# Optimization experiments

Measured on AMD Instinct MI355X. Metric: run time of the kernel, lower is better.

## Reference

```python
import jax, jax.numpy as jnp
import numpy as np

NEG = -1.0e9


def setup_inputs() -> dict:
    key = jax.random.key(0)
    ks = jax.random.split(key, 8)
    B, L, D = 4, 2048, 1024
    s = 1.0 / np.sqrt(D)
    return {
        "x": jax.random.normal(ks[0], (B, L, D), dtype=jnp.float32),
        "Wq": jax.random.normal(ks[1], (D, D), dtype=jnp.float32) * s,
        "bq": jax.random.normal(ks[2], (D,), dtype=jnp.float32) * 0.02,
        "Wk": jax.random.normal(ks[3], (D, D), dtype=jnp.float32) * s,
        "bk": jax.random.normal(ks[4], (D,), dtype=jnp.float32) * 0.02,
        "Wv": jax.random.normal(ks[5], (D, D), dtype=jnp.float32) * s,
        "bv": jax.random.normal(ks[6], (D,), dtype=jnp.float32) * 0.02,
        "lengths": jax.random.randint(ks[7], (B,), 1, 2048, dtype=jnp.int32),
    }


def reference(x, Wq, bq, Wk, bk, Wv, bv, lengths):
    # x: [B, L, D]; single-head self-attention with causal + length additive masks
    B, L, D = x.shape
    q = x @ Wq + bq  # [B, L, D]
    k = x @ Wk + bk
    v = x @ Wv + bv
    scale = 1.0 / jnp.sqrt(jnp.asarray(D, dtype=x.dtype))
    att = jnp.einsum("bid,bjd->bij", q, k) * scale  # [B, L, L]
    idx = jnp.arange(L)
    causal = jnp.where(idx[None, :] > idx[:, None], NEG, 0.0).astype(x.dtype)  # [L, L]
    # length mask: NEG where j >= len[b] or i >= len[b]
    invalid = (idx[None, :] >= lengths[:, None])  # [B, L]
    lenmask = jnp.where(invalid[:, :, None] | invalid[:, None, :], NEG, 0.0).astype(x.dtype)
    att = att + causal[None, :, :] + lenmask
    att = jax.nn.softmax(att, axis=-1)
    return jnp.einsum("bij,bjd->bid", att, v)
```

## Files before the change

kernel.cpp:

```cpp
#include <hip/hip_runtime.h>

#define NEGV (-1.0e9f)

typedef __bf16 bf16_t;
typedef __bf16 bf16x8 __attribute__((ext_vector_type(8)));
typedef __bf16 bf16x4 __attribute__((ext_vector_type(4)));
typedef float  f32x4  __attribute__((ext_vector_type(4)));

__device__ __forceinline__ void gld16(const void* g, void* l) {
    __builtin_amdgcn_global_load_lds(
        (const __attribute__((address_space(1))) void*)g,
        (__attribute__((address_space(3))) void*)l, 16, 0, 0);
}


#define MMR(AF, IB)                                                                        \
    acc[IB][0] = __builtin_amdgcn_mfma_f32_16x16x32_bf16(AF, b0, acc[IB][0], 0, 0, 0);     \
    acc[IB][1] = __builtin_amdgcn_mfma_f32_16x16x32_bf16(AF, b1, acc[IB][1], 0, 0, 0);     \
    acc[IB][2] = __builtin_amdgcn_mfma_f32_16x16x32_bf16(AF, b2, acc[IB][2], 0, 0, 0);     \
    acc[IB][3] = __builtin_amdgcn_mfma_f32_16x16x32_bf16(AF, b3, acc[IB][3], 0, 0, 0)

__device__ __forceinline__ void ml128x128(
    const bf16_t* __restrict__ A, const bf16_t* __restrict__ B,
    int ldA, int ldB, int nkt, char* smem, int tid, f32x4 acc[4][4])
{
    const int w = tid >> 6, lane = tid & 63;
    const int wm = w & 1, wn = w >> 1;
    const int l16 = lane & 15, quad = lane >> 4;

    const int g0 = 2 * (tid >> 3) + ((tid >> 2) & 1);
    const int c0 = ((tid & 3) ^ ((tid >> 3) & 3)) * 8;
    const bf16_t* pa0 = A + (size_t)g0 * ldA + c0;
    const bf16_t* pa1 = pa0 + (size_t)64 * ldA;
    const bf16_t* pb0 = B + (size_t)g0 * ldB + c0;
    const bf16_t* pb1 = pb0 + (size_t)64 * ldB;
    char* const stA = smem + (w << 10);
    char* const stB = smem + 24576 + (w << 10);

    const int rowo = (l16 >> 1) * 128 + (l16 & 1) * 64 + ((quad ^ ((l16 >> 1) & 3)) << 4);
    const char* rdA = smem + (wm << 12) + rowo;
    const char* rdB = smem + 24576 + (wn << 12) + rowo;

#define STG4(BO) do { gld16(pa0, stA + (BO)); gld16(pa1, stA + (BO) + 4096);   \
                      gld16(pb0, stB + (BO)); gld16(pb1, stB + (BO) + 4096);   \
                      pa0 += 32; pa1 += 32; pb0 += 32; pb1 += 32; } while (0)

    STG4(0);
    if (nkt > 1) {
        STG4(8192);
        asm volatile("s_waitcnt vmcnt(4)" ::: "memory");
    } else {
        asm volatile("s_waitcnt vmcnt(0)" ::: "memory");
    }
    __builtin_amdgcn_s_barrier();

    int ro = 0, so = 16384;
    for (int kt = 0; kt < nkt; ++kt) {
        const char* ra = rdA + ro;
        const char* rb = rdB + ro;
        bf16x8 a0 = *(const bf16x8*)(ra);
        bf16x8 a1 = *(const bf16x8*)(ra + 1024);
        bf16x8 a2 = *(const bf16x8*)(ra + 2048);
        bf16x8 a3 = *(const bf16x8*)(ra + 3072);
        bf16x8 b0 = *(const bf16x8*)(rb);
        bf16x8 b1 = *(const bf16x8*)(rb + 1024);
        bf16x8 b2 = *(const bf16x8*)(rb + 2048);
        bf16x8 b3 = *(const bf16x8*)(rb + 3072);
        const bool st = (kt + 2) < nkt;
        if (st) STG4(so);
        asm volatile("s_waitcnt lgkmcnt(0)" ::: "memory");
        __builtin_amdgcn_sched_barrier(0);
        __builtin_amdgcn_s_setprio(1);
        MMR(a0, 0); MMR(a1, 1); MMR(a2, 2); MMR(a3, 3);
        __builtin_amdgcn_s_setprio(0);
        if (st) asm volatile("s_waitcnt vmcnt(4)" ::: "memory");
        else    asm volatile("s_waitcnt vmcnt(0)" ::: "memory");
        __builtin_amdgcn_s_barrier();
        ro = (ro == 16384) ? 0 : (ro + 8192);
        so = (so == 16384) ? 0 : (so + 8192);
    }
#undef STG4
}

__global__ __launch_bounds__(256)
void convert_x_kernel(const float* __restrict__ x, bf16_t* __restrict__ xb)
{
    const size_t i = ((size_t)blockIdx.x * 256 + threadIdx.x) * 8;
    float4 a = *(const float4*)&x[i];
    float4 b = *(const float4*)&x[i + 4];
    bf16x8 o;
    o[0] = (bf16_t)a.x; o[1] = (bf16_t)a.y; o[2] = (bf16_t)a.z; o[3] = (bf16_t)a.w;
    o[4] = (bf16_t)b.x; o[5] = (bf16_t)b.y; o[6] = (bf16_t)b.z; o[7] = (bf16_t)b.w;
    *(bf16x8*)&xb[i] = o;
}

__global__ __launch_bounds__(256)
void transpose_w_kernel(const float* __restrict__ W0, const float* __restrict__ W1,
                        const float* __restrict__ W2, bf16_t* __restrict__ WT)
{
    __shared__ float t[32][33];
    const float* W = (blockIdx.z == 0) ? W0 : (blockIdx.z == 1) ? W1 : W2;
    bf16_t* WTz = WT + (size_t)blockIdx.z * 1024 * 1024;
    const int k0 = blockIdx.y * 32, n0 = blockIdx.x * 32;
    const int r = threadIdx.x >> 3, c4 = (threadIdx.x & 7) * 4;
    float4 v = *(const float4*)&W[(size_t)(k0 + r) * 1024 + n0 + c4];
    t[r][c4 + 0] = v.x; t[r][c4 + 1] = v.y; t[r][c4 + 2] = v.z; t[r][c4 + 3] = v.w;
    __syncthreads();
    bf16x4 o;
#pragma unroll
    for (int j = 0; j < 4; ++j) o[j] = (bf16_t)t[c4 + j][r];
    *(bf16x4*)&WTz[(size_t)(n0 + r) * 1024 + k0 + c4] = o;
}

__global__ __launch_bounds__(256)
void gemm_qk128(const bf16_t* __restrict__ A, const bf16_t* __restrict__ Bt,
                const float* __restrict__ bq, const float* __restrict__ bk,
                bf16_t* __restrict__ C, int N, int Kd)
{
    __shared__ __align__(16) char smem[49152];
    int bid = blockIdx.y * 16 + blockIdx.x;
    bid = (bid & 7) * 128 + (bid >> 3);
    const int n0 = (bid & 15) << 7;
    const int m0 = (bid >> 4) << 7;
    const int tid = threadIdx.x;

    f32x4 acc[4][4];
#pragma unroll
    for (int i = 0; i < 4; ++i)
#pragma unroll
        for (int j = 0; j < 4; ++j) acc[i][j] = (f32x4)(0.0f);

    ml128x128(A + (size_t)m0 * Kd, Bt + (size_t)n0 * Kd, Kd, Kd, Kd >> 5,
              smem, tid, acc);

    const int w = tid >> 6, lane = tid & 63;
    const int wm = w & 1, wn = w >> 1, quad = lane >> 4, l16 = lane & 15;
#pragma unroll
    for (int j = 0; j < 4; ++j) {
        const int col = n0 + wn * 64 + j * 16 + l16;
        const float bval = (col < 1024) ? bq[col] : bk[col - 1024];
#pragma unroll
        for (int i = 0; i < 4; ++i) {
            const int row = m0 + wm * 64 + i * 16 + quad * 4;
#pragma unroll
            for (int r = 0; r < 4; ++r)
                C[(size_t)(row + r) * N + col] = (bf16_t)(acc[i][j][r] + bval);
        }
    }
}

__global__ __launch_bounds__(256)
void gemm_vt128(const bf16_t* __restrict__ WvT, const bf16_t* __restrict__ xb,
                const float* __restrict__ bv, bf16_t* __restrict__ VT,
                int N, int Kd)
{
    __shared__ __align__(16) char smem[49152];
    int bid = blockIdx.y * 64 + blockIdx.x;
    bid = (bid & 7) * 64 + (bid >> 3);
    const int m0 = (bid >> 6) << 7;
    const int n0 = (bid & 63) << 7;
    const int tid = threadIdx.x;

    f32x4 acc[4][4];
#pragma unroll
    for (int i = 0; i < 4; ++i)
#pragma unroll
        for (int j = 0; j < 4; ++j) acc[i][j] = (f32x4)(0.0f);

    ml128x128(WvT + (size_t)m0 * Kd, xb + (size_t)n0 * Kd, Kd, Kd, Kd >> 5,
              smem, tid, acc);

    const int w = tid >> 6, lane = tid & 63;
    const int wm = w & 1, wn = w >> 1, quad = lane >> 4, l16 = lane & 15;
#pragma unroll
    for (int i = 0; i < 4; ++i) {
        const int row = m0 + wm * 64 + i * 16 + quad * 4;
#pragma unroll
        for (int r = 0; r < 4; ++r) {
            const float bval = bv[row + r];
#pragma unroll
            for (int j = 0; j < 4; ++j) {
                const int col = n0 + wn * 64 + j * 16 + l16;
                VT[(size_t)(row + r) * N + col] = (bf16_t)(acc[i][j][r] + bval);
            }
        }
    }
}

__global__ __launch_bounds__(256)
void scores128(const bf16_t* __restrict__ Q, const bf16_t* __restrict__ K,
               int ldq, const int* __restrict__ lengths,
               bf16_t* __restrict__ U, float2* __restrict__ stats,
               int L, int Dd, float alpha)
{
    __shared__ __align__(16) char smem[49152];
    const int b = blockIdx.z;
    const int len = lengths[b];
    int tix = (int)blockIdx.x;
    tix = (tix & 7) * 17 + (tix >> 3);
    int it = 0;
    while ((it + 1) * (it + 2) / 2 <= tix) ++it;
    const int jt = tix - it * (it + 1) / 2;
    const int m0 = it << 7, n0 = jt << 7;
    const int tid = threadIdx.x;

    f32x4 acc[4][4];
#pragma unroll
    for (int i = 0; i < 4; ++i)
#pragma unroll
        for (int j = 0; j < 4; ++j) acc[i][j] = (f32x4)(0.0f);

    const bf16_t* Qb = Q + (size_t)b * L * ldq + (size_t)m0 * ldq;
    const bf16_t* Kb = K + (size_t)b * L * ldq + (size_t)n0 * ldq;
    ml128x128(Qb, Kb, ldq, ldq, Dd >> 5, smem, tid, acc);

    const int w = tid >> 6, lane = tid & 63;
    const int wm = w & 1, wn = w >> 1, quad = lane >> 4, l16 = lane & 15;
    bf16_t* Ub = U + (size_t)b * L * L;
    float2* strow = stats + (size_t)b * L * 32;
    const int chnk = (n0 >> 6) + wn;
#pragma unroll
    for (int i = 0; i < 4; ++i) {
#pragma unroll
        for (int r = 0; r < 4; ++r) {
            const int row = m0 + wm * 64 + i * 16 + quad * 4 + r;
            float sv[4];
#pragma unroll
            for (int j = 0; j < 4; ++j) {
                const int col = n0 + wn * 64 + j * 16 + l16;
                float v = acc[i][j][r] * alpha;
                if (col > row) v += NEGV;
                if (row >= len || col >= len) v += NEGV;
                sv[j] = v;
            }
            float m = fmaxf(fmaxf(sv[0], sv[1]), fmaxf(sv[2], sv[3]));
            m = fmaxf(m, __shfl_xor(m, 1, 64));
            m = fmaxf(m, __shfl_xor(m, 2, 64));
            m = fmaxf(m, __shfl_xor(m, 4, 64));
            m = fmaxf(m, __shfl_xor(m, 8, 64));
            float ssum = 0.f;
#pragma unroll
            for (int j = 0; j < 4; ++j) {
                sv[j] = __expf(sv[j] - m);
                ssum += sv[j];
            }
            ssum += __shfl_xor(ssum, 1, 64);
            ssum += __shfl_xor(ssum, 2, 64);
            ssum += __shfl_xor(ssum, 4, 64);
            ssum += __shfl_xor(ssum, 8, 64);
#pragma unroll
            for (int j = 0; j < 4; ++j)
                Ub[(size_t)row * L + n0 + wn * 64 + j * 16 + l16] = (bf16_t)sv[j];
            if (l16 == 0) strow[(size_t)row * 32 + chnk] = make_float2(m, ssum);
        }
    }
}

__global__ __launch_bounds__(256)
void sm_finalize_norm(const float2* __restrict__ stats, bf16_t* __restrict__ U,
                      int L)
{
    __shared__ float sc[32];
    const int i = blockIdx.x;
    const int bound = ((i >> 7) + 1) << 7;
    const int nch = bound >> 6;
    const size_t base = ((size_t)blockIdx.y * L + i) * 32;
    const int t = threadIdx.x;

    if (t < 32) {
        float m_c = -3.0e38f, s_c = 0.f;
        if (t < nch) { float2 st = stats[base + t]; m_c = st.x; s_c = st.y; }
        float M = m_c;
        M = fmaxf(M, __shfl_xor(M, 1, 64));
        M = fmaxf(M, __shfl_xor(M, 2, 64));
        M = fmaxf(M, __shfl_xor(M, 4, 64));
        M = fmaxf(M, __shfl_xor(M, 8, 64));
        M = fmaxf(M, __shfl_xor(M, 16, 64));
        const float e = __expf(m_c - M);
        float d = s_c * e;
        d += __shfl_xor(d, 1, 64);
        d += __shfl_xor(d, 2, 64);
        d += __shfl_xor(d, 4, 64);
        d += __shfl_xor(d, 8, 64);
        d += __shfl_xor(d, 16, 64);
        sc[t] = e / d;
    }
    __syncthreads();

    const int j8 = t * 8;
    if (j8 < bound) {
        bf16_t* row = U + ((size_t)blockIdx.y * L + i) * L;
        bf16x8 u = *(const bf16x8*)&row[j8];
        const float c = sc[t >> 3];
        bf16x8 o;
#pragma unroll
        for (int j = 0; j < 8; ++j) o[j] = (bf16_t)((float)u[j] * c);
        *(bf16x8*)&row[j8] = o;
    }
}

__global__ __launch_bounds__(256)
void pv128(const bf16_t* __restrict__ P, int ldp,
           const bf16_t* __restrict__ VT, int ldv,
           float* __restrict__ O, int L, int Dd)
{
    __shared__ __align__(16) char smem[49152];
    const int b = blockIdx.z;
    const int bid = blockIdx.y * 8 + blockIdx.x;
    const int mt = 15 - (bid >> 3);
    const int m0 = mt << 7, n0 = (bid & 7) << 7;
    const int tid = threadIdx.x;

    f32x4 acc[4][4];
#pragma unroll
    for (int i = 0; i < 4; ++i)
#pragma unroll
        for (int j = 0; j < 4; ++j) acc[i][j] = (f32x4)(0.0f);

    const int nkt = (m0 + 128) >> 5;
    const bf16_t* Pb = P + (size_t)b * L * ldp + (size_t)m0 * ldp;
    const bf16_t* Vb = VT + (size_t)b * L + (size_t)n0 * ldv;
    ml128x128(Pb, Vb, ldp, ldv, nkt, smem, tid, acc);

    float* Ob = O + (size_t)b * L * Dd;
    const int w = tid >> 6, lane = tid & 63;
    const int wm = w & 1, wn = w >> 1, quad = lane >> 4, l16 = lane & 15;
#pragma unroll
    for (int i = 0; i < 4; ++i) {
        const int row = m0 + wm * 64 + i * 16 + quad * 4;
#pragma unroll
        for (int j = 0; j < 4; ++j) {
            const int col = n0 + wn * 64 + j * 16 + l16;
#pragma unroll
            for (int r = 0; r < 4; ++r)
                Ob[(size_t)(row + r) * Dd + col] = acc[i][j][r];
        }
    }
}

extern "C" void kernel_launch(void* const* d_in, const int* in_sizes, int n_in,
                              void* d_out, int out_size, void* d_ws, size_t ws_size,
                              hipStream_t stream)
{
    const float* x  = (const float*)d_in[0];
    const float* Wq = (const float*)d_in[1];
    const float* bq = (const float*)d_in[2];
    const float* Wk = (const float*)d_in[3];
    const float* bk = (const float*)d_in[4];
    const float* Wv = (const float*)d_in[5];
    const float* bv = (const float*)d_in[6];
    const int*  len = (const int*)d_in[7];
    float* out = (float*)d_out;

    const int B = 4, L = 2048, D = 1024;
    const int M = B * L;
    const int N2 = 2 * D;

    bf16_t* xb = (bf16_t*)d_ws;
    bf16_t* WT = xb + (size_t)M * D;
    bf16_t* QK = WT + (size_t)3 * D * D;
    bf16_t* VT = QK + (size_t)M * N2;
    bf16_t* U  = VT + (size_t)D * M;
    float2* stats = (float2*)(U + (size_t)B * L * L);

    convert_x_kernel<<<(M * D) / 2048, 256, 0, stream>>>(x, xb);

    transpose_w_kernel<<<dim3(32, 32, 3), 256, 0, stream>>>(Wq, Wk, Wv, WT);

    gemm_qk128<<<dim3(16, 64), 256, 0, stream>>>(xb, WT, bq, bk, QK, N2, D);

    gemm_vt128<<<dim3(64, 8), 256, 0, stream>>>(
        WT + (size_t)2 * D * D, xb, bv, VT, M, D);

    scores128<<<dim3(136, 1, B), 256, 0, stream>>>(
        QK, QK + 1024, N2, len, U, stats, L, D, 0.03125f);

    sm_finalize_norm<<<dim3(L, B), 256, 0, stream>>>(stats, U, L);

    pv128<<<dim3(8, 16, 4), 256, 0, stream>>>(U, L, VT, M, out, L, D);
}
```

Measured before the change: 256.3 us.

## Fuse softmax normalization into PV GEMM and merge prep/projection launches

```diff
diff --git a/kernel.cpp b/kernel.cpp
--- a/kernel.cpp
+++ b/kernel.cpp
@@ -14,11 +14,11 @@
 }
 
 
-#define MMR(AF, IB)                                                                        \
-    acc[IB][0] = __builtin_amdgcn_mfma_f32_16x16x32_bf16(AF, b0, acc[IB][0], 0, 0, 0);     \
-    acc[IB][1] = __builtin_amdgcn_mfma_f32_16x16x32_bf16(AF, b1, acc[IB][1], 0, 0, 0);     \
-    acc[IB][2] = __builtin_amdgcn_mfma_f32_16x16x32_bf16(AF, b2, acc[IB][2], 0, 0, 0);     \
-    acc[IB][3] = __builtin_amdgcn_mfma_f32_16x16x32_bf16(AF, b3, acc[IB][3], 0, 0, 0)
+#define MMR(ACC, AF, IB)                                                                     \
+    ACC[IB][0] = __builtin_amdgcn_mfma_f32_16x16x32_bf16(AF, b0, ACC[IB][0], 0, 0, 0);       \
+    ACC[IB][1] = __builtin_amdgcn_mfma_f32_16x16x32_bf16(AF, b1, ACC[IB][1], 0, 0, 0);       \
+    ACC[IB][2] = __builtin_amdgcn_mfma_f32_16x16x32_bf16(AF, b2, ACC[IB][2], 0, 0, 0);       \
+    ACC[IB][3] = __builtin_amdgcn_mfma_f32_16x16x32_bf16(AF, b3, ACC[IB][3], 0, 0, 0)
 
 __device__ __forceinline__ void ml128x128(
     const bf16_t* __restrict__ A, const bf16_t* __restrict__ B,
@@ -71,7 +71,7 @@
         asm volatile("s_waitcnt lgkmcnt(0)" ::: "memory");
         __builtin_amdgcn_sched_barrier(0);
         __builtin_amdgcn_s_setprio(1);
-        MMR(a0, 0); MMR(a1, 1); MMR(a2, 2); MMR(a3, 3);
+        MMR(acc, a0, 0); MMR(acc, a1, 1); MMR(acc, a2, 2); MMR(acc, a3, 3);
         __builtin_amdgcn_s_setprio(0);
         if (st) asm volatile("s_waitcnt vmcnt(4)" ::: "memory");
         else    asm volatile("s_waitcnt vmcnt(0)" ::: "memory");
@@ -82,106 +82,176 @@
 #undef STG4
 }
 
+__device__ __forceinline__ void ml_pv128(
+    const bf16_t* __restrict__ A, const bf16_t* __restrict__ B,
+    int ldA, int ldB, int nkt, char* smem, const float* sc ,
+    int tid, f32x4 accO[4][4])
+{
+    const int w = tid >> 6, lane = tid & 63;
+    const int wm = w & 1, wn = w >> 1;
+    const int l16 = lane & 15, quad = lane >> 4;
+
+    const int g0 = 2 * (tid >> 3) + ((tid >> 2) & 1);
+    const int c0 = ((tid & 3) ^ ((tid >> 3) & 3)) * 8;
+    const bf16_t* pa0 = A + (size_t)g0 * ldA + c0;
+    const bf16_t* pa1 = pa0 + (size_t)64 * ldA;
+    const bf16_t* pb0 = B + (size_t)g0 * ldB + c0;
+    const bf16_t* pb1 = pb0 + (size_t)64 * ldB;
+    char* const stA = smem + (w << 10);
+    char* const stB = smem + 24576 + (w << 10);
+
+    const int rowo = (l16 >> 1) * 128 + (l16 & 1) * 64 + ((quad ^ ((l16 >> 1) & 3)) << 4);
+    const char* rdA = smem + (wm << 12) + rowo;
+    const char* rdB = smem + 24576 + (wn << 12) + rowo;
+
+    f32x4 accT[4][4];
+#pragma unroll
+    for (int i = 0; i < 4; ++i)
+#pragma unroll
+        for (int j = 0; j < 4; ++j) accT[i][j] = (f32x4)(0.0f);
+
+#define STG4(BO) do { gld16(pa0, stA + (BO)); gld16(pa1, stA + (BO) + 4096);   \
+                      gld16(pb0, stB + (BO)); gld16(pb1, stB + (BO) + 4096);   \
+                      pa0 += 32; pa1 += 32; pb0 += 32; pb1 += 32; } while (0)
+
+    STG4(0);
+    if (nkt > 1) {
+        STG4(8192);
+        asm volatile("s_waitcnt vmcnt(4)" ::: "memory");
+    } else {
+        asm volatile("s_waitcnt vmcnt(0)" ::: "memory");
+    }
+    __builtin_amdgcn_s_barrier();
+
+    int ro = 0, so = 16384;
+    for (int kt = 0; kt < nkt; ++kt) {
+        const char* ra = rdA + ro;
+        const char* rb = rdB + ro;
+        bf16x8 a0 = *(const bf16x8*)(ra);
+        bf16x8 a1 = *(const bf16x8*)(ra + 1024);
+        bf16x8 a2 = *(const bf16x8*)(ra + 2048);
+        bf16x8 a3 = *(const bf16x8*)(ra + 3072);
+        bf16x8 b0 = *(const bf16x8*)(rb);
+        bf16x8 b1 = *(const bf16x8*)(rb + 1024);
+        bf16x8 b2 = *(const bf16x8*)(rb + 2048);
+        bf16x8 b3 = *(const bf16x8*)(rb + 3072);
+        const bool st = (kt + 2) < nkt;
+        if (st) STG4(so);
+        asm volatile("s_waitcnt lgkmcnt(0)" ::: "memory");
+        __builtin_amdgcn_sched_barrier(0);
+        __builtin_amdgcn_s_setprio(1);
+        MMR(accT, a0, 0); MMR(accT, a1, 1); MMR(accT, a2, 2); MMR(accT, a3, 3);
+        __builtin_amdgcn_s_setprio(0);
+        if (kt & 1) {
+            const int c = kt >> 1;
+            const float* scc = sc + c * 128 + wm * 64 + quad * 4;
+#pragma unroll
+            for (int i = 0; i < 4; ++i) {
+                f32x4 s4 = *(const f32x4*)(scc + i * 16);
+#pragma unroll
+                for (int j = 0; j < 4; ++j) {
+                    accO[i][j] += s4 * accT[i][j];
+                    accT[i][j] = (f32x4)(0.0f);
+                }
+            }
+        }
+        if (st) asm volatile("s_waitcnt vmcnt(4)" ::: "memory");
+        else    asm volatile("s_waitcnt vmcnt(0)" ::: "memory");
+        __builtin_amdgcn_s_barrier();
+        ro = (ro == 16384) ? 0 : (ro + 8192);
+        so = (so == 16384) ? 0 : (so + 8192);
+    }
+#undef STG4
+}
+
 __global__ __launch_bounds__(256)
-void convert_x_kernel(const float* __restrict__ x, bf16_t* __restrict__ xb)
-{
-    const size_t i = ((size_t)blockIdx.x * 256 + threadIdx.x) * 8;
-    float4 a = *(const float4*)&x[i];
-    float4 b = *(const float4*)&x[i + 4];
-    bf16x8 o;
-    o[0] = (bf16_t)a.x; o[1] = (bf16_t)a.y; o[2] = (bf16_t)a.z; o[3] = (bf16_t)a.w;
-    o[4] = (bf16_t)b.x; o[5] = (bf16_t)b.y; o[6] = (bf16_t)b.z; o[7] = (bf16_t)b.w;
-    *(bf16x8*)&xb[i] = o;
+void prep_kernel(const float* __restrict__ x, bf16_t* __restrict__ xb,
+                 const float* __restrict__ W0, const float* __restrict__ W1,
+                 const float* __restrict__ W2, bf16_t* __restrict__ WT)
+{
+    __shared__ float t[32][33];
+    const int bid = blockIdx.x;
+    if (bid < 4096) {
+        const size_t i = ((size_t)bid * 256 + threadIdx.x) * 8;
+        float4 a = *(const float4*)&x[i];
+        float4 b = *(const float4*)&x[i + 4];
+        bf16x8 o;
+        o[0] = (bf16_t)a.x; o[1] = (bf16_t)a.y; o[2] = (bf16_t)a.z; o[3] = (bf16_t)a.w;
+        o[4] = (bf16_t)b.x; o[5] = (bf16_t)b.y; o[6] = (bf16_t)b.z; o[7] = (bf16_t)b.w;
+        *(bf16x8*)&xb[i] = o;
+    } else {
+        const int rr = bid - 4096;
+        const int z = rr >> 10;
+        const int rem = rr & 1023;
+        const float* W = (z == 0) ? W0 : (z == 1) ? W1 : W2;
+        bf16_t* WTz = WT + (size_t)z * 1024 * 1024;
+        const int k0 = (rem >> 5) * 32, n0 = (rem & 31) * 32;
+        const int r = threadIdx.x >> 3, c4 = (threadIdx.x & 7) * 4;
+        float4 v = *(const float4*)&W[(size_t)(k0 + r) * 1024 + n0 + c4];
+        t[r][c4 + 0] = v.x; t[r][c4 + 1] = v.y; t[r][c4 + 2] = v.z; t[r][c4 + 3] = v.w;
+        __syncthreads();
+        bf16x4 o;
+#pragma unroll
+        for (int j = 0; j < 4; ++j) o[j] = (bf16_t)t[c4 + j][r];
+        *(bf16x4*)&WTz[(size_t)(n0 + r) * 1024 + k0 + c4] = o;
+    }
 }
 
 __global__ __launch_bounds__(256)
-void transpose_w_kernel(const float* __restrict__ W0, const float* __restrict__ W1,
-                        const float* __restrict__ W2, bf16_t* __restrict__ WT)
-{
-    __shared__ float t[32][33];
-    const float* W = (blockIdx.z == 0) ? W0 : (blockIdx.z == 1) ? W1 : W2;
-    bf16_t* WTz = WT + (size_t)blockIdx.z * 1024 * 1024;
-    const int k0 = blockIdx.y * 32, n0 = blockIdx.x * 32;
-    const int r = threadIdx.x >> 3, c4 = (threadIdx.x & 7) * 4;
-    float4 v = *(const float4*)&W[(size_t)(k0 + r) * 1024 + n0 + c4];
-    t[r][c4 + 0] = v.x; t[r][c4 + 1] = v.y; t[r][c4 + 2] = v.z; t[r][c4 + 3] = v.w;
-    __syncthreads();
-    bf16x4 o;
-#pragma unroll
-    for (int j = 0; j < 4; ++j) o[j] = (bf16_t)t[c4 + j][r];
-    *(bf16x4*)&WTz[(size_t)(n0 + r) * 1024 + k0 + c4] = o;
-}
-
-__global__ __launch_bounds__(256)
-void gemm_qk128(const bf16_t* __restrict__ A, const bf16_t* __restrict__ Bt,
-                const float* __restrict__ bq, const float* __restrict__ bk,
-                bf16_t* __restrict__ C, int N, int Kd)
+void proj_kernel(const bf16_t* __restrict__ xb, const bf16_t* __restrict__ WT,
+                 const float* __restrict__ bq, const float* __restrict__ bk,
+                 const float* __restrict__ bv,
+                 bf16_t* __restrict__ QK, bf16_t* __restrict__ VT,
+                 int N2, int M, int Kd)
 {
     __shared__ __align__(16) char smem[49152];
-    int bid = blockIdx.y * 16 + blockIdx.x;
-    bid = (bid & 7) * 128 + (bid >> 3);
-    const int n0 = (bid & 15) << 7;
-    const int m0 = (bid >> 4) << 7;
     const int tid = threadIdx.x;
-
     f32x4 acc[4][4];
 #pragma unroll
     for (int i = 0; i < 4; ++i)
 #pragma unroll
         for (int j = 0; j < 4; ++j) acc[i][j] = (f32x4)(0.0f);
-
-    ml128x128(A + (size_t)m0 * Kd, Bt + (size_t)n0 * Kd, Kd, Kd, Kd >> 5,
-              smem, tid, acc);
 
     const int w = tid >> 6, lane = tid & 63;
     const int wm = w & 1, wn = w >> 1, quad = lane >> 4, l16 = lane & 15;
-#pragma unroll
-    for (int j = 0; j < 4; ++j) {
-        const int col = n0 + wn * 64 + j * 16 + l16;
-        const float bval = (col < 1024) ? bq[col] : bk[col - 1024];
+
+    if ((int)blockIdx.x < 1024) {
+        int bid = blockIdx.x;
+        bid = (bid & 7) * 128 + (bid >> 3);
+        const int n0 = (bid & 15) << 7;
+        const int m0 = (bid >> 4) << 7;
+        ml128x128(xb + (size_t)m0 * Kd, WT + (size_t)n0 * Kd, Kd, Kd, Kd >> 5,
+                  smem, tid, acc);
+#pragma unroll
+        for (int j = 0; j < 4; ++j) {
+            const int col = n0 + wn * 64 + j * 16 + l16;
+            const float bval = (col < 1024) ? bq[col] : bk[col - 1024];
+#pragma unroll
+            for (int i = 0; i < 4; ++i) {
+                const int row = m0 + wm * 64 + i * 16 + quad * 4;
+#pragma unroll
+                for (int r = 0; r < 4; ++r)
+                    QK[(size_t)(row + r) * N2 + col] = (bf16_t)(acc[i][j][r] + bval);
+            }
+        }
+    } else {
+        int bid = blockIdx.x - 1024;
+        bid = (bid & 7) * 64 + (bid >> 3);
+        const int m0 = (bid >> 6) << 7;
+        const int n0 = (bid & 63) << 7;
+        ml128x128(WT + (size_t)2 * Kd * Kd + (size_t)m0 * Kd,
+                  xb + (size_t)n0 * Kd, Kd, Kd, Kd >> 5, smem, tid, acc);
 #pragma unroll
         for (int i = 0; i < 4; ++i) {
             const int row = m0 + wm * 64 + i * 16 + quad * 4;
 #pragma unroll
-            for (int r = 0; r < 4; ++r)
-                C[(size_t)(row + r) * N + col] = (bf16_t)(acc[i][j][r] + bval);
-        }
-    }
-}
-
-__global__ __launch_bounds__(256)
-void gemm_vt128(const bf16_t* __restrict__ WvT, const bf16_t* __restrict__ xb,
-                const float* __restrict__ bv, bf16_t* __restrict__ VT,
-                int N, int Kd)
-{
-    __shared__ __align__(16) char smem[49152];
-    int bid = blockIdx.y * 64 + blockIdx.x;
-    bid = (bid & 7) * 64 + (bid >> 3);
-    const int m0 = (bid >> 6) << 7;
-    const int n0 = (bid & 63) << 7;
-    const int tid = threadIdx.x;
-
-    f32x4 acc[4][4];
-#pragma unroll
-    for (int i = 0; i < 4; ++i)
-#pragma unroll
-        for (int j = 0; j < 4; ++j) acc[i][j] = (f32x4)(0.0f);
-
-    ml128x128(WvT + (size_t)m0 * Kd, xb + (size_t)n0 * Kd, Kd, Kd, Kd >> 5,
-              smem, tid, acc);
-
-    const int w = tid >> 6, lane = tid & 63;
-    const int wm = w & 1, wn = w >> 1, quad = lane >> 4, l16 = lane & 15;
-#pragma unroll
-    for (int i = 0; i < 4; ++i) {
-        const int row = m0 + wm * 64 + i * 16 + quad * 4;
-#pragma unroll
-        for (int r = 0; r < 4; ++r) {
-            const float bval = bv[row + r];
-#pragma unroll
-            for (int j = 0; j < 4; ++j) {
-                const int col = n0 + wn * 64 + j * 16 + l16;
-                VT[(size_t)(row + r) * N + col] = (bf16_t)(acc[i][j][r] + bval);
+            for (int r = 0; r < 4; ++r) {
+                const float bval = bv[row + r];
+#pragma unroll
+                for (int j = 0; j < 4; ++j) {
+                    const int col = n0 + wn * 64 + j * 16 + l16;
+                    VT[(size_t)(row + r) * M + col] = (bf16_t)(acc[i][j][r] + bval);
+                }
             }
         }
     }
@@ -257,70 +327,57 @@
 }
 
 __global__ __launch_bounds__(256)
-void sm_finalize_norm(const float2* __restrict__ stats, bf16_t* __restrict__ U,
-                      int L)
-{
-    __shared__ float sc[32];
-    const int i = blockIdx.x;
-    const int bound = ((i >> 7) + 1) << 7;
-    const int nch = bound >> 6;
-    const size_t base = ((size_t)blockIdx.y * L + i) * 32;
-    const int t = threadIdx.x;
-
-    if (t < 32) {
-        float m_c = -3.0e38f, s_c = 0.f;
-        if (t < nch) { float2 st = stats[base + t]; m_c = st.x; s_c = st.y; }
-        float M = m_c;
-        M = fmaxf(M, __shfl_xor(M, 1, 64));
-        M = fmaxf(M, __shfl_xor(M, 2, 64));
-        M = fmaxf(M, __shfl_xor(M, 4, 64));
-        M = fmaxf(M, __shfl_xor(M, 8, 64));
-        M = fmaxf(M, __shfl_xor(M, 16, 64));
-        const float e = __expf(m_c - M);
-        float d = s_c * e;
-        d += __shfl_xor(d, 1, 64);
-        d += __shfl_xor(d, 2, 64);
-        d += __shfl_xor(d, 4, 64);
-        d += __shfl_xor(d, 8, 64);
-        d += __shfl_xor(d, 16, 64);
-        sc[t] = e / d;
-    }
-    __syncthreads();
-
-    const int j8 = t * 8;
-    if (j8 < bound) {
-        bf16_t* row = U + ((size_t)blockIdx.y * L + i) * L;
-        bf16x8 u = *(const bf16x8*)&row[j8];
-        const float c = sc[t >> 3];
-        bf16x8 o;
-#pragma unroll
-        for (int j = 0; j < 8; ++j) o[j] = (bf16_t)((float)u[j] * c);
-        *(bf16x8*)&row[j8] = o;
-    }
-}
-
-__global__ __launch_bounds__(256)
-void pv128(const bf16_t* __restrict__ P, int ldp,
+void pv128(const bf16_t* __restrict__ U, int ldp,
+           const float2* __restrict__ stats,
            const bf16_t* __restrict__ VT, int ldv,
            float* __restrict__ O, int L, int Dd)
 {
-    __shared__ __align__(16) char smem[49152];
+    __shared__ __align__(16) char smem[49152 + 32 * 128 * 4];
+    float* sc = (float*)(smem + 49152);
     const int b = blockIdx.z;
     const int bid = blockIdx.y * 8 + blockIdx.x;
     const int mt = 15 - (bid >> 3);
     const int m0 = mt << 7, n0 = (bid & 7) << 7;
     const int tid = threadIdx.x;
 
-    f32x4 acc[4][4];
+    {
+        const int row = tid >> 1;
+        const int half = tid & 1;
+        const int nch = (m0 + 128) >> 6;
+        const float2* st = stats + ((size_t)b * L + m0 + row) * 32 + half * 16;
+        float mloc[16], sloc[16];
+        float mmax = -3.0e38f;
+#pragma unroll
+        for (int c = 0; c < 16; ++c) {
+            const int ch = half * 16 + c;
+            float2 v = (ch < nch) ? st[c] : make_float2(-3.0e38f, 0.f);
+            mloc[c] = v.x; sloc[c] = v.y;
+            mmax = fmaxf(mmax, v.x);
+        }
+        const float M = fmaxf(mmax, __shfl_xor(mmax, 1, 64));
+        float d = 0.f;
+#pragma unroll
+        for (int c = 0; c < 16; ++c) d += sloc[c] * __expf(mloc[c] - M);
+        d += __shfl_xor(d, 1, 64);
+        const float invD = 1.0f / d;
+#pragma unroll
+        for (int c = 0; c < 16; ++c) {
+            const int ch = half * 16 + c;
+            if (ch < nch) sc[ch * 128 + row] = __expf(mloc[c] - M) * invD;
+        }
+    }
+    __syncthreads();
+
+    f32x4 accO[4][4];
 #pragma unroll
     for (int i = 0; i < 4; ++i)
 #pragma unroll
-        for (int j = 0; j < 4; ++j) acc[i][j] = (f32x4)(0.0f);
+        for (int j = 0; j < 4; ++j) accO[i][j] = (f32x4)(0.0f);
 
     const int nkt = (m0 + 128) >> 5;
-    const bf16_t* Pb = P + (size_t)b * L * ldp + (size_t)m0 * ldp;
+    const bf16_t* Pb = U + (size_t)b * L * ldp + (size_t)m0 * ldp;
     const bf16_t* Vb = VT + (size_t)b * L + (size_t)n0 * ldv;
-    ml128x128(Pb, Vb, ldp, ldv, nkt, smem, tid, acc);
+    ml_pv128(Pb, Vb, ldp, ldv, nkt, smem, sc, tid, accO);
 
     float* Ob = O + (size_t)b * L * Dd;
     const int w = tid >> 6, lane = tid & 63;
@@ -333,7 +390,7 @@
             const int col = n0 + wn * 64 + j * 16 + l16;
 #pragma unroll
             for (int r = 0; r < 4; ++r)
-                Ob[(size_t)(row + r) * Dd + col] = acc[i][j][r];
+                Ob[(size_t)(row + r) * Dd + col] = accO[i][j][r];
         }
     }
 }
@@ -363,19 +420,12 @@
     bf16_t* U  = VT + (size_t)D * M;
     float2* stats = (float2*)(U + (size_t)B * L * L);
 
-    convert_x_kernel<<<(M * D) / 2048, 256, 0, stream>>>(x, xb);
-
-    transpose_w_kernel<<<dim3(32, 32, 3), 256, 0, stream>>>(Wq, Wk, Wv, WT);
-
-    gemm_qk128<<<dim3(16, 64), 256, 0, stream>>>(xb, WT, bq, bk, QK, N2, D);
-
-    gemm_vt128<<<dim3(64, 8), 256, 0, stream>>>(
-        WT + (size_t)2 * D * D, xb, bv, VT, M, D);
+    prep_kernel<<<7168, 256, 0, stream>>>(x, xb, Wq, Wk, Wv, WT);
+
+    proj_kernel<<<1536, 256, 0, stream>>>(xb, WT, bq, bk, bv, QK, VT, N2, M, D);
 
     scores128<<<dim3(136, 1, B), 256, 0, stream>>>(
         QK, QK + 1024, N2, len, U, stats, L, D, 0.03125f);
 
-    sm_finalize_norm<<<dim3(L, B), 256, 0, stream>>>(stats, U, L);
-
-    pv128<<<dim3(8, 16, 4), 256, 0, stream>>>(U, L, VT, M, out, L, D);
-}
+    pv128<<<dim3(8, 16, 4), 256, 0, stream>>>(U, L, stats, VT, M, out, L, D);
+}
```

Result: no change. 260.2 us (+1.5%).
